# Kernel tuning notes

Hardware: AMD Instinct MI355X
Metric: run time of the kernel (lower is better)

The kernel has to match this reference:

```python
import jax, jax.numpy as jnp
import numpy as np

N = 50000      # total nodes
E = 500000     # edges
D = 128        # in_channels
B = 50         # graphs in batch
NPG = N // B   # nodes per graph (equal-sized graphs)
RATIO = 0.5
ALPHA = 0.6


def setup_inputs() -> dict:
    key = jax.random.key(0)
    ks = jax.random.split(key, 8)
    x = jax.random.normal(ks[0], (N, D), dtype=jnp.float32)
    edge_index = jax.random.randint(ks[1], (2, E), 0, N, dtype=jnp.int32)
    batch = jnp.repeat(jnp.arange(B, dtype=jnp.int32), NPG)  # sorted, equal blocks
    s = 1.0 / np.sqrt(D)
    # GCNConv(D,1) for structure score
    W_s = jax.random.normal(ks[2], (D, 1), dtype=jnp.float32) * s
    b_s = jnp.zeros((1,), dtype=jnp.float32)
    # Linear(D,1) for feature score
    W_f = jax.random.normal(ks[3], (1, D), dtype=jnp.float32) * s
    b_f = jnp.zeros((1,), dtype=jnp.float32)
    # GCNConv(D,D) fusion layer
    W_fu = jax.random.normal(ks[4], (D, D), dtype=jnp.float32) * s
    b_fu = jnp.zeros((D,), dtype=jnp.float32)
    return {"x": x, "edge_index": edge_index, "batch": batch,
            "W_s": W_s, "b_s": b_s, "W_f": W_f, "b_f": b_f,
            "W_fu": W_fu, "b_fu": b_fu}


def gcn_conv(x, src, dst, W, b, n):
    """PyG GCNConv: add self loops, symmetric D^-1/2 (A+I) D^-1/2 @ (xW) + b."""
    xw = x @ W                                  # [n, out]
    loop = jnp.arange(n, dtype=src.dtype)
    s = jnp.concatenate([src, loop])
    d = jnp.concatenate([dst, loop])
    deg = jax.ops.segment_sum(jnp.ones_like(s, dtype=xw.dtype), d, num_segments=n)
    dinv = jax.lax.rsqrt(jnp.maximum(deg, 1e-12))
    norm = dinv[s] * dinv[d]                    # [E+n]
    out = jax.ops.segment_sum(norm[:, None] * xw[s], d, num_segments=n)
    return out + b


def reference(x, edge_index, batch, W_s, b_s, W_f, b_f, W_fu, b_fu):
    src, dst = edge_index[0], edge_index[1]
    # fused score: alpha * structure (GCN) + (1-alpha) * feature (Linear)
    score_s = gcn_conv(x, src, dst, W_s, b_s, N)[:, 0]          # [N]
    score_f = (x @ W_f.T + b_f)[:, 0]                           # [N]
    score = jnp.tanh(ALPHA * score_s + (1.0 - ALPHA) * score_f)
    # per-graph top-k (equal-sized graphs -> dense [B, NPG] view, like the torch topk)
    k = int(np.ceil(RATIO * NPG))
    dense = score.reshape(B, NPG)
    order = jnp.argsort(-dense, axis=-1)                        # descending
    offsets = (jnp.arange(B, dtype=jnp.int32) * NPG)[:, None]
    perm = (order[:, :k].astype(jnp.int32) + offsets).reshape(-1)  # [B*k]
    # fusion conv on full graph, then gather selected nodes
    x_fused = gcn_conv(x, src, dst, W_fu, b_fu, N)              # [N, D]
    x_ae = x_fused[perm]                                        # [B*k, D]
    x_out = x_ae * score[perm][:, None]                         # multiplier == 1
    batch_out = batch[perm]
    # filter_adj: remap node ids, keep edges with both endpoints selected
    nodemap = jnp.full((N,), -1, dtype=jnp.int32).at[perm].set(
        jnp.arange(perm.shape[0], dtype=jnp.int32))
    r, c = nodemap[src], nodemap[dst]
    m = (r >= 0) & (c >= 0)
    edge_index_new = jnp.stack([r[m], c[m]], axis=0)
    return (x_out, edge_index_new, batch_out, perm, x_ae)
```

## Files before the change

### kernel.cpp

```cpp
#include <hip/hip_runtime.h>
#include <math.h>

#define N_NODES 50000
#define N_EDGES 500000
#define DIM     128
#define NGRAPH  50
#define NPGC    1000
#define KSEL    500
#define SORT_N  1024
#define NBE     489
#define NBN     49
#define GEMM_BLKS 782
#define DEG_BLKS  1954
#define DOTS_BLKS 12500
#define NDINV     196
#define GATH_BLKS 6250
#define NREP    8


__global__ __launch_bounds__(256) void k1_gemm_deg(const float* __restrict__ x,
                                                   const float* __restrict__ W,
                                                   float* __restrict__ xw,
                                                   const int* __restrict__ dst,
                                                   int* __restrict__ degrep,
                                                   int* __restrict__ eslot) {
    __shared__ float lds[12288];
    int t = threadIdx.x;
    if (blockIdx.x >= GEMM_BLKS) {
        int e = (blockIdx.x - GEMM_BLKS) * 256 + t;
        if (e < N_EDGES) {
            int d = dst[e];
            int r = e & (NREP - 1);
            int old = atomicAdd(&degrep[r * N_NODES + d], 1);
            eslot[e] = (old << 3) | r;
        }
        return;
    }
    float* Wt = lds;
    float* Xt = lds + 64 * DIM;
    int cg = t & 15;
    int ng = t >> 4;
    int node_base = blockIdx.x * 64;

    float4 acc[4][2];
    #pragma unroll
    for (int nn = 0; nn < 4; nn++) {
        acc[nn][0] = make_float4(0.f, 0.f, 0.f, 0.f);
        acc[nn][1] = make_float4(0.f, 0.f, 0.f, 0.f);
    }
    for (int half = 0; half < 2; half++) {
        const float4* Wg = (const float4*)(W + half * 64 * DIM);
        float4* Wl = (float4*)Wt;
        #pragma unroll
        for (int i = 0; i < 8; i++) {
            int f = t + i * 256;
            Wl[f] = Wg[f];
        }
        #pragma unroll
        for (int i = 0; i < 4; i++) {
            int f = t + i * 256;
            int row = f >> 4, col = f & 15;
            int node = node_base + row;
            float4 v = make_float4(0.f, 0.f, 0.f, 0.f);
            if (node < N_NODES) v = *(const float4*)&x[(size_t)node * DIM + half * 64 + col * 4];
            *(float4*)&Xt[(row << 6) + ((col ^ (row & 15)) << 2)] = v;
        }
        __syncthreads();
        #pragma unroll 2
        for (int kc = 0; kc < 16; kc++) {
            int k = kc << 2;
            float4 wa[4], wb[4];
            #pragma unroll
            for (int kk = 0; kk < 4; kk++) {
                wa[kk] = *(const float4*)&Wt[(k + kk) * DIM + (cg << 2)];
                wb[kk] = *(const float4*)&Wt[(k + kk) * DIM + (cg << 2) + 64];
            }
            int csw = (kc ^ ng) << 2;
            #pragma unroll
            for (int nn = 0; nn < 4; nn++) {
                float4 xv = *(const float4*)&Xt[((ng + (nn << 4)) << 6) + csw];
                acc[nn][0].x += xv.x * wa[0].x + xv.y * wa[1].x + xv.z * wa[2].x + xv.w * wa[3].x;
                acc[nn][0].y += xv.x * wa[0].y + xv.y * wa[1].y + xv.z * wa[2].y + xv.w * wa[3].y;
                acc[nn][0].z += xv.x * wa[0].z + xv.y * wa[1].z + xv.z * wa[2].z + xv.w * wa[3].z;
                acc[nn][0].w += xv.x * wa[0].w + xv.y * wa[1].w + xv.z * wa[2].w + xv.w * wa[3].w;
                acc[nn][1].x += xv.x * wb[0].x + xv.y * wb[1].x + xv.z * wb[2].x + xv.w * wb[3].x;
                acc[nn][1].y += xv.x * wb[0].y + xv.y * wb[1].y + xv.z * wb[2].y + xv.w * wb[3].y;
                acc[nn][1].z += xv.x * wb[0].z + xv.y * wb[1].z + xv.z * wb[2].z + xv.w * wb[3].z;
                acc[nn][1].w += xv.x * wb[0].w + xv.y * wb[1].w + xv.z * wb[2].w + xv.w * wb[3].w;
            }
        }
        __syncthreads();
    }
    #pragma unroll
    for (int nn = 0; nn < 4; nn++) {
        int node = node_base + ng + (nn << 4);
        if (node < N_NODES) {
            *(float4*)&xw[(size_t)node * DIM + (cg << 2)]      = acc[nn][0];
            *(float4*)&xw[(size_t)node * DIM + (cg << 2) + 64] = acc[nn][1];
        }
    }
}


__global__ __launch_bounds__(256) void k2_dots_scan_dinv(const int* __restrict__ degrep,
                                                         int* __restrict__ repoff,
                                                         int* __restrict__ deg,
                                                         int* __restrict__ rowoff,
                                                         int* __restrict__ bsumsN,
                                                         const float* __restrict__ x,
                                                         const float* __restrict__ Ws,
                                                         const float* __restrict__ Wf,
                                                         const float* __restrict__ bf,
                                                         double* __restrict__ pack,
                                                         float* __restrict__ dinvf,
                                                         double* __restrict__ sf) {
    int t = threadIdx.x;
    int lane = t & 63, wid = t >> 6;
    int bid = blockIdx.x;
    if (bid < DOTS_BLKS) {
        int node = bid * 4 + wid;
        const float* xr = x + (size_t)node * DIM;
        double x1 = (double)xr[lane], x2 = (double)xr[lane + 64];
        double ps = x1 * (double)Ws[lane] + x2 * (double)Ws[lane + 64];
        double pf = x1 * (double)Wf[lane] + x2 * (double)Wf[lane + 64];
        for (int off = 32; off > 0; off >>= 1) {
            ps += __shfl_down(ps, off, 64);
            pf += __shfl_down(pf, off, 64);
        }
        if (lane == 0) {
            pack[2 * node + 1] = ps;
            sf[node] = pf + (double)bf[0];
        }
        return;
    }
    if (bid < DOTS_BLKS + NBN) {
        __shared__ int ws4[4];
        int base = (bid - DOTS_BLKS) * 1024 + t * 4;
        int v0 = 0, v1 = 0, v2 = 0, v3 = 0;
        if (base < N_NODES) {
            #pragma unroll
            for (int r = 0; r < NREP; r++) {
                int4 vv = *(const int4*)&degrep[r * N_NODES + base];
                v0 += vv.x; v1 += vv.y; v2 += vv.z; v3 += vv.w;
            }
        }
        int s4 = v0 + v1 + v2 + v3;
        int incl = s4;
        #pragma unroll
        for (int off = 1; off < 64; off <<= 1) {
            int u = __shfl_up(incl, off, 64);
            if (lane >= off) incl += u;
        }
        if (lane == 63) ws4[wid] = incl;
        __syncthreads();
        int woff = 0;
        #pragma unroll
        for (int w = 0; w < 4; w++) if (w < wid) woff += ws4[w];
        int excl = incl - s4 + woff;
        if (base + 0 < N_NODES) rowoff[base + 0] = excl;
        if (base + 1 < N_NODES) rowoff[base + 1] = excl + v0;
        if (base + 2 < N_NODES) rowoff[base + 2] = excl + v0 + v1;
        if (base + 3 < N_NODES) rowoff[base + 3] = excl + v0 + v1 + v2;
        if (t == 255) bsumsN[bid - DOTS_BLKS] = woff + incl;
        return;
    }
    int i = (bid - DOTS_BLKS - NBN) * 256 + t;
    if (i < N_NODES) {
        int o = 0;
        #pragma unroll
        for (int r = 0; r < NREP; r++) {
            int c = degrep[r * N_NODES + i];
            repoff[r * N_NODES + i] = o;
            o += c;
        }
        deg[i] = o;
        double di = 1.0 / sqrt((double)(o + 1));
        pack[2 * i] = di;
        dinvf[i] = (float)di;
    }
}


__global__ __launch_bounds__(256) void k3_csr(const int* __restrict__ src,
                                              const int* __restrict__ dst,
                                              const int* __restrict__ rowoff,
                                              const int* __restrict__ bsumsN,
                                              const int* __restrict__ repoff,
                                              const int* __restrict__ eslot,
                                              int* __restrict__ csr) {
    __shared__ int bsN[64];
    int t = threadIdx.x;
    if (t < 64) {
        int v = (t < NBN) ? bsumsN[t] : 0;
        int incl = v;
        #pragma unroll
        for (int off = 1; off < 64; off <<= 1) {
            int u = __shfl_up(incl, off, 64);
            if (t >= off) incl += u;
        }
        bsN[t] = incl - v;
    }
    __syncthreads();
    int e = blockIdx.x * 256 + t;
    if (e >= N_EDGES) return;
    int d = dst[e];
    int es = eslot[e];
    int r = es & (NREP - 1), slot = es >> 3;
    int pos = rowoff[d] + bsN[d >> 10] + repoff[r * N_NODES + d] + slot;
    csr[pos] = src[e];
}


__global__ __launch_bounds__(256) void k3b_score(const int* __restrict__ csr,
                                                 const int* __restrict__ rowoff,
                                                 const int* __restrict__ bsumsN,
                                                 const int* __restrict__ deg,
                                                 const double* __restrict__ pack,
                                                 double* __restrict__ score_sd) {
    __shared__ int bsN[64];
    int t = threadIdx.x;
    if (t < 64) {
        int v = (t < NBN) ? bsumsN[t] : 0;
        int incl = v;
        #pragma unroll
        for (int off = 1; off < 64; off <<= 1) {
            int u = __shfl_up(incl, off, 64);
            if (t >= off) incl += u;
        }
        bsN[t] = incl - v;
    }
    __syncthreads();
    int node = blockIdx.x * 256 + t;
    if (node >= N_NODES) return;
    int base = rowoff[node] + bsN[node >> 10];
    int cnt  = deg[node];
    double acc0 = 0.0, acc1 = 0.0;
    int i = 0;
    for (; i + 2 <= cnt; i += 2) {
        int s0 = csr[base + i];
        int s1 = csr[base + i + 1];
        double2 p0 = ((const double2*)pack)[s0];
        double2 p1 = ((const double2*)pack)[s1];
        acc0 += p0.x * p0.y;
        acc1 += p1.x * p1.y;
    }
    if (i < cnt) {
        int s0 = csr[base + i];
        double2 p0 = ((const double2*)pack)[s0];
        acc0 += p0.x * p0.y;
    }
    score_sd[node] = pack[2 * node] * (acc0 + acc1);
}


__global__ __launch_bounds__(512) void k4_topk(const double* __restrict__ score_sd,
                                               const double* __restrict__ pack,
                                               const double* __restrict__ sf,
                                               const float* __restrict__ bs,
                                               const int* __restrict__ batch,
                                               int* __restrict__ perm, int* __restrict__ nodemap,
                                               float* __restrict__ scoref_sel,
                                               float* __restrict__ out, long o2, long o3) {
    __shared__ double key[SORT_N];
    __shared__ int    idx[SORT_N];
    int g = blockIdx.x, t = threadIdx.x;
    const double A = 0.6, OMA = 1.0 - 0.6;
    double bsv = (double)bs[0];
    for (int i = t; i < SORT_N; i += 512) {
        if (i < NPGC) {
            int node = g * NPGC + i;
            double2 p = ((const double2*)pack)[node];
            double tot = score_sd[node] + p.x * p.x * p.y + bsv;
            key[i] = tanh(A * tot + OMA * sf[node]);
            idx[i] = i;
        } else { key[i] = -1e300; idx[i] = i; }
    }
    __syncthreads();
    for (int size = 2; size <= SORT_N; size <<= 1) {
        for (int stride = size >> 1; stride > 0; stride >>= 1) {
            int a = ((t & ~(stride - 1)) << 1) | (t & (stride - 1));
            int b = a | stride;
            bool descFirst = ((a & size) == 0);
            double ka = key[a], kb = key[b];
            int ia = idx[a], ib = idx[b];
            bool aAfterB = (ka < kb) || (ka == kb && ia > ib);
            if (descFirst ? aAfterB : !aAfterB) {
                key[a] = kb; key[b] = ka;
                idx[a] = ib; idx[b] = ia;
            }
            __syncthreads();
        }
    }
    for (int j = t; j < KSEL; j += 512) {
        int node = g * NPGC + idx[j];
        int pos  = g * KSEL + j;
        perm[pos]        = node;
        nodemap[node]    = pos + 1;
        scoref_sel[pos]  = (float)key[j];
        out[o2 + pos]    = (float)batch[node];
        out[o3 + pos]    = (float)node;
    }
}


__global__ __launch_bounds__(256) void k5_escan_gather(const int* __restrict__ src,
                                                       const int* __restrict__ dst,
                                                       const int* __restrict__ nodemap,
                                                       int* __restrict__ epos,
                                                       int* __restrict__ bsumsE,
                                                       const float* __restrict__ xw,
                                                       const int* __restrict__ perm,
                                                       const int* __restrict__ rowoff,
                                                       const int* __restrict__ bsumsN,
                                                       const int* __restrict__ deg,
                                                       const int* __restrict__ csr,
                                                       const float* __restrict__ dinvf,
                                                       const float* __restrict__ scoref_sel,
                                                       const float* __restrict__ b_fu,
                                                       float* __restrict__ out, long o4) {
    int t = threadIdx.x;
    int lane = t & 63, wid = t >> 6;
    if (blockIdx.x < NBE) {
        __shared__ int ws4[4];
        int base = blockIdx.x * 1024 + t * 4;
        int v0 = 0, v1 = 0, v2 = 0, v3 = 0;
        if (base + 0 < N_EDGES) v0 = (nodemap[src[base + 0]] > 0 && nodemap[dst[base + 0]] > 0);
        if (base + 1 < N_EDGES) v1 = (nodemap[src[base + 1]] > 0 && nodemap[dst[base + 1]] > 0);
        if (base + 2 < N_EDGES) v2 = (nodemap[src[base + 2]] > 0 && nodemap[dst[base + 2]] > 0);
        if (base + 3 < N_EDGES) v3 = (nodemap[src[base + 3]] > 0 && nodemap[dst[base + 3]] > 0);
        int s4 = v0 + v1 + v2 + v3;
        int incl = s4;
        #pragma unroll
        for (int off = 1; off < 64; off <<= 1) {
            int u = __shfl_up(incl, off, 64);
            if (lane >= off) incl += u;
        }
        if (lane == 63) ws4[wid] = incl;
        __syncthreads();
        int woff = 0;
        #pragma unroll
        for (int w = 0; w < 4; w++) if (w < wid) woff += ws4[w];
        int excl = incl - s4 + woff;
        if (base + 0 < N_EDGES) epos[base + 0] = excl;
        if (base + 1 < N_EDGES) epos[base + 1] = excl + v0;
        if (base + 2 < N_EDGES) epos[base + 2] = excl + v0 + v1;
        if (base + 3 < N_EDGES) epos[base + 3] = excl + v0 + v1 + v2;
        if (t == 255) bsumsE[blockIdx.x] = woff + incl;
        return;
    }
    __shared__ int bsN[64];
    if (t < 64) {
        int v = (t < NBN) ? bsumsN[t] : 0;
        int incl = v;
        #pragma unroll
        for (int off = 1; off < 64; off <<= 1) {
            int u = __shfl_up(incl, off, 64);
            if (t >= off) incl += u;
        }
        bsN[t] = incl - v;
    }
    __syncthreads();
    int wave = (blockIdx.x - NBE) * 4 + wid;
    int p = perm[wave];
    float dpf = dinvf[p];
    int c2 = lane * 2;
    float2 v = ((const float2*)(xw + (size_t)p * DIM))[lane];
    float nself = dpf * dpf;
    float ax = nself * v.x, ay = nself * v.y;
    int beg = rowoff[p] + bsN[p >> 10], cnt = deg[p];
    int i = 0;
    for (; i + 2 <= cnt; i += 2) {
        int s0 = csr[beg + i];
        int s1 = csr[beg + i + 1];
        float2 u0 = ((const float2*)(xw + (size_t)s0 * DIM))[lane];
        float2 u1 = ((const float2*)(xw + (size_t)s1 * DIM))[lane];
        float n0 = dinvf[s0] * dpf, n1 = dinvf[s1] * dpf;
        ax += n0 * u0.x; ay += n0 * u0.y;
        ax += n1 * u1.x; ay += n1 * u1.y;
    }
    if (i < cnt) {
        int s0 = csr[beg + i];
        float2 u0 = ((const float2*)(xw + (size_t)s0 * DIM))[lane];
        float n0 = dinvf[s0] * dpf;
        ax += n0 * u0.x; ay += n0 * u0.y;
    }
    ax += b_fu[c2];
    ay += b_fu[c2 + 1];
    float sc = scoref_sel[wave];
    size_t ro = (size_t)wave * DIM + c2;
    out[o4 + ro]     = ax;
    out[o4 + ro + 1] = ay;
    out[ro]          = ax * sc;
    out[ro + 1]      = ay * sc;
}


__global__ __launch_bounds__(256) void k6_compact(const int* __restrict__ src,
                                                  const int* __restrict__ dst,
                                                  const int* __restrict__ nodemap,
                                                  const int* __restrict__ epos,
                                                  const int* __restrict__ bsumsE,
                                                  float* __restrict__ out_edges, long M) {
    __shared__ int bsE[512];
    int t = threadIdx.x;
    if (t < 64) {
        int carry = 0;
        #pragma unroll
        for (int c = 0; c < 8; c++) {
            int i = c * 64 + t;
            int v = (i < NBE) ? bsumsE[i] : 0;
            int incl = v;
            #pragma unroll
            for (int off = 1; off < 64; off <<= 1) {
                int u = __shfl_up(incl, off, 64);
                if (t >= off) incl += u;
            }
            if (i < 512) bsE[i] = incl - v + carry;
            carry += __shfl(incl, 63, 64);
        }
    }
    __syncthreads();
    int e = blockIdx.x * 256 + t;
    if (e >= N_EDGES) return;
    int r = nodemap[src[e]], c = nodemap[dst[e]];
    if (r > 0 && c > 0) {
        int pos = epos[e] + bsE[e >> 10];
        out_edges[pos]     = (float)(r - 1);
        out_edges[M + pos] = (float)(c - 1);
    }
}


extern "C" void kernel_launch(void* const* d_in, const int* in_sizes, int n_in,
                              void* d_out, int out_size, void* d_ws, size_t ws_size,
                              hipStream_t stream) {
    const float* x    = (const float*)d_in[0];
    const int*   ei   = (const int*)d_in[1];
    const int*   src  = ei;
    const int*   dst  = ei + N_EDGES;
    const int*   batch= (const int*)d_in[2];
    const float* W_s  = (const float*)d_in[3];
    const float* b_s  = (const float*)d_in[4];
    const float* W_f  = (const float*)d_in[5];
    const float* b_f  = (const float*)d_in[6];
    const float* W_fu = (const float*)d_in[7];
    const float* b_fu = (const float*)d_in[8];
    float* out = (float*)d_out;

    char* wsp = (char*)d_ws;
    size_t off = 0;
    auto take = [&](size_t bytes) -> char* {
        char* p = wsp + off;
        off = (off + bytes + 255) & ~(size_t)255;
        return p;
    };
    char*   zbase      = wsp;
    int*    degrep     = (int*)   take((size_t)NREP * N_NODES * 4);
    int*    nodemap    = (int*)   take((size_t)N_NODES * 4);
    size_t  zbytes     = off;
    int*    repoff     = (int*)   take((size_t)NREP * N_NODES * 4);
    int*    eslot      = (int*)   take((size_t)N_EDGES * 4);
    int*    deg        = (int*)   take((size_t)N_NODES * 4);
    double* score_sd   = (double*)take((size_t)N_NODES * 8);
    double* pack       = (double*)take((size_t)N_NODES * 16);
    double* sf         = (double*)take((size_t)N_NODES * 8);
    float*  dinvf      = (float*) take((size_t)N_NODES * 4);
    float*  scoref_sel = (float*) take((size_t)NGRAPH * KSEL * 4);
    int*    perm       = (int*)   take((size_t)NGRAPH * KSEL * 4);
    int*    rowoff     = (int*)   take((size_t)N_NODES * 4);
    int*    epos       = (int*)   take((size_t)N_EDGES * 4);
    int*    bsumsE     = (int*)   take((size_t)1024 * 4);
    int*    bsumsN     = (int*)   take((size_t)1024 * 4);
    int*    csr        = (int*)   take((size_t)N_EDGES * 4);
    float*  xw         = (float*) take((size_t)N_NODES * DIM * 4);

    long M  = ((long)out_size - 6450000L) / 2;
    long o1 = 3200000L;
    long o2 = o1 + 2 * M;
    long o3 = o2 + (long)NGRAPH * KSEL;
    long o4 = o3 + (long)NGRAPH * KSEL;

    hipMemsetAsync(zbase, 0, zbytes, stream);

    k1_gemm_deg<<<GEMM_BLKS + DEG_BLKS, 256, 0, stream>>>(x, W_fu, xw, dst, degrep, eslot);
    k2_dots_scan_dinv<<<DOTS_BLKS + NBN + NDINV, 256, 0, stream>>>(degrep, repoff, deg,
                                                                   rowoff, bsumsN,
                                                                   x, W_s, W_f, b_f,
                                                                   pack, dinvf, sf);
    k3_csr<<<DEG_BLKS, 256, 0, stream>>>(src, dst, rowoff, bsumsN, repoff, eslot, csr);
    k3b_score<<<NDINV, 256, 0, stream>>>(csr, rowoff, bsumsN, deg, pack, score_sd);
    k4_topk<<<NGRAPH, 512, 0, stream>>>(score_sd, pack, sf, b_s, batch,
                                        perm, nodemap, scoref_sel, out, o2, o3);
    k5_escan_gather<<<NBE + GATH_BLKS, 256, 0, stream>>>(src, dst, nodemap, epos, bsumsE,
                                                         xw, perm, rowoff, bsumsN, deg, csr,
                                                         dinvf, scoref_sel, b_fu, out, o4);
    k6_compact<<<DEG_BLKS, 256, 0, stream>>>(src, dst, nodemap, epos, bsumsE, out + o1, M);
}
```

Measured before the change: 220.9 us.

## Use per-block private degree histograms with workgroup-scope atomics for CSR build

```diff
diff --git a/kernel.cpp b/kernel.cpp
--- a/kernel.cpp
+++ b/kernel.cpp
@@ -9,30 +9,38 @@
 #define KSEL    500
 #define SORT_N  1024
 #define NBE     489
-#define NBN     49
 #define GEMM_BLKS 782
-#define DEG_BLKS  1954
+#define EDGE_BLKS 1954
 #define DOTS_BLKS 12500
 #define NDINV     196
 #define GATH_BLKS 6250
-#define NREP    8
+#define DEGB    64
+#define NCHUNK  1954
 
 
 __global__ __launch_bounds__(256) void k1_gemm_deg(const float* __restrict__ x,
                                                    const float* __restrict__ W,
                                                    float* __restrict__ xw,
                                                    const int* __restrict__ dst,
-                                                   int* __restrict__ degrep,
+                                                   int* __restrict__ degpriv,
                                                    int* __restrict__ eslot) {
     __shared__ float lds[12288];
     int t = threadIdx.x;
-    if (blockIdx.x >= GEMM_BLKS) {
-        int e = (blockIdx.x - GEMM_BLKS) * 256 + t;
-        if (e < N_EDGES) {
-            int d = dst[e];
-            int r = e & (NREP - 1);
-            int old = atomicAdd(&degrep[r * N_NODES + d], 1);
-            eslot[e] = (old << 3) | r;
+    if (blockIdx.x < DEGB) {
+        int b = blockIdx.x;
+        int* priv = degpriv + b * N_NODES;
+        for (int c = b; c < NCHUNK; c += 2 * DEGB) {
+            int e1 = (c << 8) + t;
+            int cB = c + DEGB;
+            int e2 = (cB << 8) + t;
+            int d1 = (e1 < N_EDGES) ? dst[e1] : -1;
+            int d2 = (cB < NCHUNK && e2 < N_EDGES) ? dst[e2] : -1;
+            if (d1 >= 0)
+                eslot[e1] = __hip_atomic_fetch_add(&priv[d1], 1, __ATOMIC_RELAXED,
+                                                   __HIP_MEMORY_SCOPE_WORKGROUP);
+            if (d2 >= 0)
+                eslot[e2] = __hip_atomic_fetch_add(&priv[d2], 1, __ATOMIC_RELAXED,
+                                                   __HIP_MEMORY_SCOPE_WORKGROUP);
         }
         return;
     }
@@ -40,7 +48,7 @@
     float* Xt = lds + 64 * DIM;
     int cg = t & 15;
     int ng = t >> 4;
-    int node_base = blockIdx.x * 64;
+    int node_base = (blockIdx.x - DEGB) * 64;
 
     float4 acc[4][2];
     #pragma unroll
@@ -102,18 +110,17 @@
 }
 
 
-__global__ __launch_bounds__(256) void k2_dots_scan_dinv(const int* __restrict__ degrep,
-                                                         int* __restrict__ repoff,
-                                                         int* __restrict__ deg,
-                                                         int* __restrict__ rowoff,
-                                                         int* __restrict__ bsumsN,
-                                                         const float* __restrict__ x,
-                                                         const float* __restrict__ Ws,
-                                                         const float* __restrict__ Wf,
-                                                         const float* __restrict__ bf,
-                                                         double* __restrict__ pack,
-                                                         float* __restrict__ dinvf,
-                                                         double* __restrict__ sf) {
+__global__ __launch_bounds__(256) void k2_dots_merge(int* __restrict__ degpriv,
+                                                     int* __restrict__ deg,
+                                                     int* __restrict__ rowoff,
+                                                     int* __restrict__ bsums256,
+                                                     const float* __restrict__ x,
+                                                     const float* __restrict__ Ws,
+                                                     const float* __restrict__ Wf,
+                                                     const float* __restrict__ bf,
+                                                     double* __restrict__ pack,
+                                                     float* __restrict__ dinvf,
+                                                     double* __restrict__ sf) {
     int t = threadIdx.x;
     int lane = t & 63, wid = t >> 6;
     int bid = blockIdx.x;
@@ -133,44 +140,14 @@
         }
         return;
     }
-    if (bid < DOTS_BLKS + NBN) {
-        __shared__ int ws4[4];
-        int base = (bid - DOTS_BLKS) * 1024 + t * 4;
-        int v0 = 0, v1 = 0, v2 = 0, v3 = 0;
-        if (base < N_NODES) {
-            #pragma unroll
-            for (int r = 0; r < NREP; r++) {
-                int4 vv = *(const int4*)&degrep[r * N_NODES + base];
-                v0 += vv.x; v1 += vv.y; v2 += vv.z; v3 += vv.w;
-            }
-        }
-        int s4 = v0 + v1 + v2 + v3;
-        int incl = s4;
-        #pragma unroll
-        for (int off = 1; off < 64; off <<= 1) {
-            int u = __shfl_up(incl, off, 64);
-            if (lane >= off) incl += u;
-        }
-        if (lane == 63) ws4[wid] = incl;
-        __syncthreads();
-        int woff = 0;
-        #pragma unroll
-        for (int w = 0; w < 4; w++) if (w < wid) woff += ws4[w];
-        int excl = incl - s4 + woff;
-        if (base + 0 < N_NODES) rowoff[base + 0] = excl;
-        if (base + 1 < N_NODES) rowoff[base + 1] = excl + v0;
-        if (base + 2 < N_NODES) rowoff[base + 2] = excl + v0 + v1;
-        if (base + 3 < N_NODES) rowoff[base + 3] = excl + v0 + v1 + v2;
-        if (t == 255) bsumsN[bid - DOTS_BLKS] = woff + incl;
-        return;
-    }
-    int i = (bid - DOTS_BLKS - NBN) * 256 + t;
+    int i = (bid - DOTS_BLKS) * 256 + t;
+    int o = 0;
     if (i < N_NODES) {
-        int o = 0;
-        #pragma unroll
-        for (int r = 0; r < NREP; r++) {
-            int c = degrep[r * N_NODES + i];
-            repoff[r * N_NODES + i] = o;
+        #pragma unroll 8
+        for (int b = 0; b < DEGB; b++) {
+            int* p = &degpriv[b * N_NODES + i];
+            int c = *p;
+            *p = o;
             o += c;
         }
         deg[i] = o;
@@ -178,61 +155,86 @@
         pack[2 * i] = di;
         dinvf[i] = (float)di;
     }
+    __shared__ int ws4[4];
+    int incl = o;
+    #pragma unroll
+    for (int off = 1; off < 64; off <<= 1) {
+        int u = __shfl_up(incl, off, 64);
+        if (lane >= off) incl += u;
+    }
+    if (lane == 63) ws4[wid] = incl;
+    __syncthreads();
+    int woff = 0;
+    #pragma unroll
+    for (int w = 0; w < 4; w++) if (w < wid) woff += ws4[w];
+    if (i < N_NODES) rowoff[i] = incl - o + woff;
+    if (t == 255) bsums256[bid - DOTS_BLKS] = woff + incl;
 }
 
 
 __global__ __launch_bounds__(256) void k3_csr(const int* __restrict__ src,
                                               const int* __restrict__ dst,
                                               const int* __restrict__ rowoff,
-                                              const int* __restrict__ bsumsN,
-                                              const int* __restrict__ repoff,
+                                              const int* __restrict__ bsums256,
+                                              const int* __restrict__ degpriv,
                                               const int* __restrict__ eslot,
                                               int* __restrict__ csr) {
-    __shared__ int bsN[64];
+    __shared__ int bsN[256];
     int t = threadIdx.x;
     if (t < 64) {
-        int v = (t < NBN) ? bsumsN[t] : 0;
-        int incl = v;
-        #pragma unroll
-        for (int off = 1; off < 64; off <<= 1) {
-            int u = __shfl_up(incl, off, 64);
-            if (t >= off) incl += u;
-        }
-        bsN[t] = incl - v;
+        int carry = 0;
+        #pragma unroll
+        for (int ch = 0; ch < 4; ch++) {
+            int i = ch * 64 + t;
+            int v = (i < NDINV) ? bsums256[i] : 0;
+            int incl = v;
+            #pragma unroll
+            for (int off = 1; off < 64; off <<= 1) {
+                int u = __shfl_up(incl, off, 64);
+                if (t >= off) incl += u;
+            }
+            bsN[i] = incl - v + carry;
+            carry += __shfl(incl, 63, 64);
+        }
     }
     __syncthreads();
     int e = blockIdx.x * 256 + t;
     if (e >= N_EDGES) return;
     int d = dst[e];
-    int es = eslot[e];
-    int r = es & (NREP - 1), slot = es >> 3;
-    int pos = rowoff[d] + bsN[d >> 10] + repoff[r * N_NODES + d] + slot;
+    int owner = (e >> 8) & (DEGB - 1);
+    int pos = rowoff[d] + bsN[d >> 8] + degpriv[owner * N_NODES + d] + eslot[e];
     csr[pos] = src[e];
 }
 
 
 __global__ __launch_bounds__(256) void k3b_score(const int* __restrict__ csr,
                                                  const int* __restrict__ rowoff,
-                                                 const int* __restrict__ bsumsN,
+                                                 const int* __restrict__ bsums256,
                                                  const int* __restrict__ deg,
                                                  const double* __restrict__ pack,
                                                  double* __restrict__ score_sd) {
-    __shared__ int bsN[64];
+    __shared__ int bsN[256];
     int t = threadIdx.x;
     if (t < 64) {
-        int v = (t < NBN) ? bsumsN[t] : 0;
-        int incl = v;
-        #pragma unroll
-        for (int off = 1; off < 64; off <<= 1) {
-            int u = __shfl_up(incl, off, 64);
-            if (t >= off) incl += u;
-        }
-        bsN[t] = incl - v;
+        int carry = 0;
+        #pragma unroll
+        for (int ch = 0; ch < 4; ch++) {
+            int i = ch * 64 + t;
+            int v = (i < NDINV) ? bsums256[i] : 0;
+            int incl = v;
+            #pragma unroll
+            for (int off = 1; off < 64; off <<= 1) {
+                int u = __shfl_up(incl, off, 64);
+                if (t >= off) incl += u;
+            }
+            bsN[i] = incl - v + carry;
+            carry += __shfl(incl, 63, 64);
+        }
     }
     __syncthreads();
     int node = blockIdx.x * 256 + t;
     if (node >= N_NODES) return;
-    int base = rowoff[node] + bsN[node >> 10];
+    int base = rowoff[node] + bsN[node >> 8];
     int cnt  = deg[node];
     double acc0 = 0.0, acc1 = 0.0;
     int i = 0;
@@ -311,7 +313,7 @@
                                                        const float* __restrict__ xw,
                                                        const int* __restrict__ perm,
                                                        const int* __restrict__ rowoff,
-                                                       const int* __restrict__ bsumsN,
+                                                       const int* __restrict__ bsums256,
                                                        const int* __restrict__ deg,
                                                        const int* __restrict__ csr,
                                                        const float* __restrict__ dinvf,
@@ -348,16 +350,22 @@
         if (t == 255) bsumsE[blockIdx.x] = woff + incl;
         return;
     }
-    __shared__ int bsN[64];
+    __shared__ int bsN[256];
     if (t < 64) {
-        int v = (t < NBN) ? bsumsN[t] : 0;
-        int incl = v;
-        #pragma unroll
-        for (int off = 1; off < 64; off <<= 1) {
-            int u = __shfl_up(incl, off, 64);
-            if (t >= off) incl += u;
-        }
-        bsN[t] = incl - v;
+        int carry = 0;
+        #pragma unroll
+        for (int ch = 0; ch < 4; ch++) {
+            int i = ch * 64 + t;
+            int v = (i < NDINV) ? bsums256[i] : 0;
+            int incl = v;
+            #pragma unroll
+            for (int off = 1; off < 64; off <<= 1) {
+                int u = __shfl_up(incl, off, 64);
+                if (t >= off) incl += u;
+            }
+            bsN[i] = incl - v + carry;
+            carry += __shfl(incl, 63, 64);
+        }
     }
     __syncthreads();
     int wave = (blockIdx.x - NBE) * 4 + wid;
@@ -367,7 +375,7 @@
     float2 v = ((const float2*)(xw + (size_t)p * DIM))[lane];
     float nself = dpf * dpf;
     float ax = nself * v.x, ay = nself * v.y;
-    int beg = rowoff[p] + bsN[p >> 10], cnt = deg[p];
+    int beg = rowoff[p] + bsN[p >> 8], cnt = deg[p];
     int i = 0;
     for (; i + 2 <= cnt; i += 2) {
         int s0 = csr[beg + i];
@@ -455,10 +463,9 @@
         return p;
     };
     char*   zbase      = wsp;
-    int*    degrep     = (int*)   take((size_t)NREP * N_NODES * 4);
+    int*    degpriv    = (int*)   take((size_t)DEGB * N_NODES * 4);
     int*    nodemap    = (int*)   take((size_t)N_NODES * 4);
     size_t  zbytes     = off;
-    int*    repoff     = (int*)   take((size_t)NREP * N_NODES * 4);
     int*    eslot      = (int*)   take((size_t)N_EDGES * 4);
     int*    deg        = (int*)   take((size_t)N_NODES * 4);
     double* score_sd   = (double*)take((size_t)N_NODES * 8);
@@ -470,7 +477,7 @@
     int*    rowoff     = (int*)   take((size_t)N_NODES * 4);
     int*    epos       = (int*)   take((size_t)N_EDGES * 4);
     int*    bsumsE     = (int*)   take((size_t)1024 * 4);
-    int*    bsumsN     = (int*)   take((size_t)1024 * 4);
+    int*    bsums256   = (int*)   take((size_t)1024 * 4);
     int*    csr        = (int*)   take((size_t)N_EDGES * 4);
     float*  xw         = (float*) take((size_t)N_NODES * DIM * 4);
 
@@ -482,17 +489,16 @@
 
     hipMemsetAsync(zbase, 0, zbytes, stream);
 
-    k1_gemm_deg<<<GEMM_BLKS + DEG_BLKS, 256, 0, stream>>>(x, W_fu, xw, dst, degrep, eslot);
-    k2_dots_scan_dinv<<<DOTS_BLKS + NBN + NDINV, 256, 0, stream>>>(degrep, repoff, deg,
-                                                                   rowoff, bsumsN,
-                                                                   x, W_s, W_f, b_f,
-                                                                   pack, dinvf, sf);
-    k3_csr<<<DEG_BLKS, 256, 0, stream>>>(src, dst, rowoff, bsumsN, repoff, eslot, csr);
-    k3b_score<<<NDINV, 256, 0, stream>>>(csr, rowoff, bsumsN, deg, pack, score_sd);
+    k1_gemm_deg<<<DEGB + GEMM_BLKS, 256, 0, stream>>>(x, W_fu, xw, dst, degpriv, eslot);
+    k2_dots_merge<<<DOTS_BLKS + NDINV, 256, 0, stream>>>(degpriv, deg, rowoff, bsums256,
+                                                         x, W_s, W_f, b_f,
+                                                         pack, dinvf, sf);
+    k3_csr<<<EDGE_BLKS, 256, 0, stream>>>(src, dst, rowoff, bsums256, degpriv, eslot, csr);
+    k3b_score<<<NDINV, 256, 0, stream>>>(csr, rowoff, bsums256, deg, pack, score_sd);
     k4_topk<<<NGRAPH, 512, 0, stream>>>(score_sd, pack, sf, b_s, batch,
                                         perm, nodemap, scoref_sel, out, o2, o3);
     k5_escan_gather<<<NBE + GATH_BLKS, 256, 0, stream>>>(src, dst, nodemap, epos, bsumsE,
-                                                         xw, perm, rowoff, bsumsN, deg, csr,
+                                                         xw, perm, rowoff, bsums256, deg, csr,
                                                          dinvf, scoref_sel, b_fu, out, o4);
-    k6_compact<<<DEG_BLKS, 256, 0, stream>>>(src, dst, nodemap, epos, bsumsE, out + o1, M);
-}
+    k6_compact<<<EDGE_BLKS, 256, 0, stream>>>(src, dst, nodemap, epos, bsumsE, out + o1, M);
+}
```

Result: no change. 223.7 us (+1.3%).
